# Optimization experiments

Hardware: AMD Instinct MI355X
Metric: run time of the kernel (lower is better)

## Reference

```python
import jax, jax.numpy as jnp
import numpy as np

IN, H, B = 1024, 1024, 8192
EPS = 1e-5

def _ln(x, g, b):
    mu = jnp.mean(x, axis=-1, keepdims=True)
    var = jnp.mean(jnp.square(x - mu), axis=-1, keepdims=True)
    return (x - mu) * jax.lax.rsqrt(var + EPS) * g + b

def setup_inputs() -> dict:
    key = jax.random.key(0)
    ks = jax.random.split(key, 6)
    inp = {
        "input": jax.random.normal(ks[0], (B, IN), dtype=jnp.float32),
        "h_prev": jax.random.normal(ks[1], (B, H), dtype=jnp.float32),
        "c_prev": jax.random.normal(ks[2], (B, H), dtype=jnp.float32),
        # Linear(in, 4H, bias=False) weights, stored [out, in] like torch
        "w_i": jax.random.normal(ks[3], (4 * H, IN), dtype=jnp.float32) / np.sqrt(IN),
        "w_h": jax.random.normal(ks[4], (4 * H, H), dtype=jnp.float32) / np.sqrt(H),
    }
    for name in ("ln_i", "ln_h", "ln_g", "ln_o", "ln_c"):
        inp[name + "_g"] = jnp.ones((H,), dtype=jnp.float32)
        inp[name + "_b"] = jnp.zeros((H,), dtype=jnp.float32)
    return inp

def reference(input, h_prev, c_prev, w_i, w_h,
              ln_i_g, ln_i_b, ln_h_g, ln_h_b, ln_g_g, ln_g_b,
              ln_o_g, ln_o_b, ln_c_g, ln_c_b):
    gi = input @ w_i.T            # [B, 4H]
    gh = h_prev @ w_h.T           # [B, 4H]
    i_i, i_f, i_gc, i_o = jnp.split(gi, 4, axis=-1)
    h_i, h_f, h_g, h_o = jnp.split(gh, 4, axis=-1)
    i_g = jax.nn.sigmoid(_ln(i_i + h_i, ln_i_g, ln_i_b))
    f_g = jax.nn.sigmoid(_ln(i_f + h_f, ln_h_g, ln_h_b))
    # NOTE: faithful to source bug — uses sigmoided i_g (not chunk i_gc) here
    g_g = jnp.tanh(_ln(i_g + h_g, ln_g_g, ln_g_b))
    o_g = jax.nn.sigmoid(_ln(i_o + h_o, ln_o_g, ln_o_b))
    c_new = _ln(f_g * c_prev + i_g * g_g, ln_c_g, ln_c_b)
    h_new = o_g * jnp.tanh(c_new)
    return (h_new, c_new)
```

## Files before the change

### kernel.cpp

```cpp
#include <hip/hip_runtime.h>
#include <hip/hip_bf16.h>

#define BATCH 8192
#define HDIM  1024
#define KDIM  2048
#define NDIM  4096

__device__ inline unsigned short f2bf(float x) {
    unsigned int u = __float_as_uint(x);
    unsigned int r = (u + 0x7fffu + ((u >> 16) & 1u)) >> 16;
    return (unsigned short)r;
}
__device__ inline float bf2f(unsigned short u) {
    return __uint_as_float((unsigned int)u << 16);
}

__global__ __launch_bounds__(256) void convert_kernel(
    const float* __restrict__ wi, const float* __restrict__ wh,
    const float* __restrict__ input, const float* __restrict__ h_prev,
    unsigned short* __restrict__ Wb, unsigned short* __restrict__ Xb)
{
    int idx = blockIdx.x * 256 + threadIdx.x;
    const int NW = NDIM * 512;
    float4 v;
    unsigned short* dst;
    if (idx < NW) {
        int n = idx >> 9;
        int k = (idx & 511) << 2;
        if (k < 1024) {
            if (n >= 2048 && n < 3072) v = make_float4(0.f, 0.f, 0.f, 0.f);
            else                       v = *(const float4*)(wi + (size_t)n * 1024 + k);
        } else {
            v = *(const float4*)(wh + (size_t)n * 1024 + (k - 1024));
        }
        dst = Wb + (size_t)n * KDIM + k;
    } else {
        int j = idx - NW;
        int r = j >> 9;
        int k = (j & 511) << 2;
        if (k < 1024) v = *(const float4*)(input  + (size_t)r * 1024 + k);
        else          v = *(const float4*)(h_prev + (size_t)r * 1024 + (k - 1024));
        dst = Xb + (size_t)r * KDIM + k;
    }
    ushort4 o;
    o.x = f2bf(v.x); o.y = f2bf(v.y); o.z = f2bf(v.z); o.w = f2bf(v.w);
    *(ushort4*)dst = o;
}

#define BM 256
#define BN 128
#define BK 64

typedef __attribute__((ext_vector_type(8))) short bf16x8;
typedef __attribute__((ext_vector_type(4))) float f32x4;

__global__ __launch_bounds__(512) void gemm_bt_kernel(
    const unsigned short* __restrict__ A,
    const unsigned short* __restrict__ Bw,
    unsigned short* __restrict__ G,
    int M)
{
    __shared__ unsigned short As[BM * BK];
    __shared__ unsigned short Bs[BN * BK];

    const int tid  = threadIdx.x;
    const int lane = tid & 63;
    const int wave = tid >> 6;

    const int bid = blockIdx.x;
    const int bm  = (bid >> 5) * BM;
    const int bn  = (bid & 31) * BN;

    f32x4 acc[4][4] = {};

    const int wm = (wave >> 1) * 64;
    const int wn = (wave & 1) * 64;

    const int srow = lane >> 3;
    const int c_sw = (lane & 7) ^ srow;

    int k0 = 0;
    if (bn >= 2048 && bn < 3072) k0 = 1024;

    for (; k0 < KDIM; k0 += BK) {
#pragma unroll
        for (int p = 0; p < 4; ++p) {
            const int rbase = wave * 32 + p * 8;
            const unsigned short* gA =
                A + (size_t)(bm + rbase + srow) * KDIM + k0 + c_sw * 8;
            __builtin_amdgcn_global_load_lds(
                (const __attribute__((address_space(1))) void*)gA,
                (__attribute__((address_space(3))) void*)&As[rbase * BK], 16, 0, 0);
        }
#pragma unroll
        for (int p = 0; p < 2; ++p) {
            const int rbase = wave * 16 + p * 8;
            const unsigned short* gB =
                Bw + (size_t)(bn + rbase + srow) * KDIM + k0 + c_sw * 8;
            __builtin_amdgcn_global_load_lds(
                (const __attribute__((address_space(1))) void*)gB,
                (__attribute__((address_space(3))) void*)&Bs[rbase * BK], 16, 0, 0);
        }
        __syncthreads();

#pragma unroll
        for (int kk = 0; kk < 2; ++kk) {
            bf16x8 af[4], bfr[4];
            const int cbase = kk * 4 + (lane >> 4);
#pragma unroll
            for (int i = 0; i < 4; ++i) {
                const int ra = wm + i * 16 + (lane & 15);
                af[i]  = *(const bf16x8*)&As[ra * BK + ((cbase ^ (ra & 7)) * 8)];
                const int rb = wn + i * 16 + (lane & 15);
                bfr[i] = *(const bf16x8*)&Bs[rb * BK + ((cbase ^ (rb & 7)) * 8)];
            }
#pragma unroll
            for (int i = 0; i < 4; ++i)
#pragma unroll
                for (int j = 0; j < 4; ++j)
                    acc[i][j] = __builtin_amdgcn_mfma_f32_16x16x32_bf16(
                        af[i], bfr[j], acc[i][j], 0, 0, 0);
        }
        __syncthreads();
    }

#pragma unroll
    for (int i = 0; i < 4; ++i) {
#pragma unroll
        for (int j = 0; j < 4; ++j) {
#pragma unroll
            for (int r = 0; r < 4; ++r) {
                int row = bm + wm + i * 16 + (lane >> 4) * 4 + r;
                int col = bn + wn + j * 16 + (lane & 15);
                G[(size_t)row * NDIM + col] = f2bf(acc[i][j][r]);
            }
        }
    }
}

__device__ inline float sigmoid_f(float x) { return 1.f / (1.f + __expf(-x)); }
__device__ inline float tanh_f(float x) { return 1.f - 2.f / (__expf(2.f * x) + 1.f); }

typedef __attribute__((ext_vector_type(8))) unsigned short us8;

__device__ inline void wstats(const float* x, float& mu, float& rs)
{
    float s = 0.f, q = 0.f;
#pragma unroll
    for (int e = 0; e < 16; ++e) { s += x[e]; q += x[e] * x[e]; }
#pragma unroll
    for (int o = 1; o < 64; o <<= 1) {
        s += __shfl_xor(s, o);
        q += __shfl_xor(q, o);
    }
    mu = s * (1.f / 1024.f);
    float var = q * (1.f / 1024.f) - mu * mu;
    rs = rsqrtf(var + 1e-5f);
}

#define LOADG16(dst, basep)                                            \
    _Pragma("unroll")                                                  \
    for (int j = 0; j < 2; ++j) {                                      \
        us8 t = *(const us8*)((basep) + j * 512 + cbase);              \
        _Pragma("unroll")                                              \
        for (int e = 0; e < 8; ++e) dst[j * 8 + e] = bf2f(t[e]);       \
    }

#define LOADF16(dst, basep)                                            \
    _Pragma("unroll")                                                  \
    for (int j = 0; j < 2; ++j) {                                      \
        float4 a = *(const float4*)((basep) + j * 512 + cbase);        \
        float4 b = *(const float4*)((basep) + j * 512 + cbase + 4);    \
        dst[j * 8 + 0] = a.x; dst[j * 8 + 1] = a.y;                    \
        dst[j * 8 + 2] = a.z; dst[j * 8 + 3] = a.w;                    \
        dst[j * 8 + 4] = b.x; dst[j * 8 + 5] = b.y;                    \
        dst[j * 8 + 6] = b.z; dst[j * 8 + 7] = b.w;                    \
    }

__global__ __launch_bounds__(256) void lstm_ew_kernel(
    const unsigned short* __restrict__ G,
    const float* __restrict__ c_prev,
    const float* __restrict__ p0g, const float* __restrict__ p0b,
    const float* __restrict__ p1g, const float* __restrict__ p1b,
    const float* __restrict__ p2g, const float* __restrict__ p2b,
    const float* __restrict__ p3g, const float* __restrict__ p3b,
    const float* __restrict__ p4g, const float* __restrict__ p4b,
    float* __restrict__ out_h, float* __restrict__ out_c,
    int row_base)
{
    const int lane  = threadIdx.x & 63;
    const int wave  = threadIdx.x >> 6;
    const int r     = blockIdx.x * 4 + wave;
    const int grow  = row_base + r;
    const int cbase = lane * 8;

    const unsigned short* Grow = G + (size_t)r * NDIM;

    float tmp[16], pg[16], pb[16];
    float ig[16], cm[16], og[16];
    float mu, rs;

    LOADG16(tmp, Grow);
    wstats(tmp, mu, rs);
    LOADF16(pg, p0g); LOADF16(pb, p0b);
#pragma unroll
    for (int e = 0; e < 16; ++e)
        ig[e] = sigmoid_f((tmp[e] - mu) * rs * pg[e] + pb[e]);

    LOADG16(tmp, Grow + 1024);
    wstats(tmp, mu, rs);
    LOADF16(pg, p1g); LOADF16(pb, p1b);
    LOADF16(cm, c_prev + (size_t)grow * HDIM);
#pragma unroll
    for (int e = 0; e < 16; ++e)
        cm[e] *= sigmoid_f((tmp[e] - mu) * rs * pg[e] + pb[e]);

    LOADG16(tmp, Grow + 2048);
#pragma unroll
    for (int e = 0; e < 16; ++e) tmp[e] += ig[e];
    wstats(tmp, mu, rs);
    LOADF16(pg, p2g); LOADF16(pb, p2b);
#pragma unroll
    for (int e = 0; e < 16; ++e)
        cm[e] += ig[e] * tanh_f((tmp[e] - mu) * rs * pg[e] + pb[e]);

    LOADG16(tmp, Grow + 3072);
    wstats(tmp, mu, rs);
    LOADF16(pg, p3g); LOADF16(pb, p3b);
#pragma unroll
    for (int e = 0; e < 16; ++e)
        og[e] = sigmoid_f((tmp[e] - mu) * rs * pg[e] + pb[e]);

    wstats(cm, mu, rs);
    LOADF16(pg, p4g); LOADF16(pb, p4b);
    float cn[16], hn[16];
#pragma unroll
    for (int e = 0; e < 16; ++e) {
        cn[e] = (cm[e] - mu) * rs * pg[e] + pb[e];
        hn[e] = og[e] * tanh_f(cn[e]);
    }

    float* oh = out_h + (size_t)grow * HDIM;
    float* oc = out_c + (size_t)grow * HDIM;
#pragma unroll
    for (int j = 0; j < 2; ++j) {
        *(float4*)(oh + j * 512 + cbase) =
            make_float4(hn[j*8+0], hn[j*8+1], hn[j*8+2], hn[j*8+3]);
        *(float4*)(oh + j * 512 + cbase + 4) =
            make_float4(hn[j*8+4], hn[j*8+5], hn[j*8+6], hn[j*8+7]);
        *(float4*)(oc + j * 512 + cbase) =
            make_float4(cn[j*8+0], cn[j*8+1], cn[j*8+2], cn[j*8+3]);
        *(float4*)(oc + j * 512 + cbase + 4) =
            make_float4(cn[j*8+4], cn[j*8+5], cn[j*8+6], cn[j*8+7]);
    }
}

extern "C" void kernel_launch(void* const* d_in, const int* in_sizes, int n_in,
                              void* d_out, int out_size, void* d_ws, size_t ws_size,
                              hipStream_t stream)
{
    const float* input  = (const float*)d_in[0];
    const float* h_prev = (const float*)d_in[1];
    const float* c_prev = (const float*)d_in[2];
    const float* w_i    = (const float*)d_in[3];
    const float* w_h    = (const float*)d_in[4];
    const float* lng[10];
    for (int i = 0; i < 10; ++i) lng[i] = (const float*)d_in[5 + i];

    unsigned short* Xb = (unsigned short*)d_ws;
    size_t xb_bytes = (size_t)BATCH * KDIM * 2;
    unsigned short* Wb = (unsigned short*)((char*)d_ws + xb_bytes);
    size_t wb_bytes = (size_t)NDIM * KDIM * 2;
    unsigned short* G = (unsigned short*)((char*)d_ws + xb_bytes + wb_bytes);

    size_t g_avail = (ws_size > xb_bytes + wb_bytes) ? (ws_size - xb_bytes - wb_bytes) : 0;
    long max_rows = (long)(g_avail / ((size_t)NDIM * sizeof(unsigned short)));
    int chunk = (max_rows >= BATCH) ? BATCH : (int)((max_rows / BM) * BM);
    if (chunk <= 0) chunk = BM;

    convert_kernel<<<(NDIM * 512 + BATCH * 512) / 256, 256, 0, stream>>>(
        w_i, w_h, input, h_prev, Wb, Xb);

    float* out_h = (float*)d_out;
    float* out_c = out_h + (size_t)BATCH * HDIM;

    for (int rb = 0; rb < BATCH; rb += chunk) {
        int rows = (BATCH - rb < chunk) ? (BATCH - rb) : chunk;
        gemm_bt_kernel<<<(rows / BM) * (NDIM / BN), 512, 0, stream>>>(
            Xb + (size_t)rb * KDIM, Wb, G, rows);
        lstm_ew_kernel<<<rows / 4, 256, 0, stream>>>(
            G, c_prev, lng[0], lng[1], lng[2], lng[3], lng[4],
            lng[5], lng[6], lng[7], lng[8], lng[9], out_h, out_c, rb);
    }
}
```

Before: 330.7 us.

## Double-buffer GEMM LDS tiles, widen block tile to 256x256, prioritize MFMA phases

Restructures the bf16 GEMM main loop so global-to-LDS loads for the next K tile are issued into a second LDS buffer while the current tile is computed, with an explicit vmcnt wait and raw barriers. This hides global load latency behind MFMA work. The block tile grows from 256x128 to 256x256, with each wave computing a 128x64 sub-tile to raise operand reuse. Fragment loads are interleaved with MFMA groups under s_setprio. The cost is 128KB of LDS per block, a larger accumulator register footprint and half as many blocks, which lowers occupancy and the parallelism available across CUs.

```diff
diff --git a/kernel.cpp b/kernel.cpp
--- a/kernel.cpp
+++ b/kernel.cpp
@@ -48,11 +48,83 @@
 }
 
 #define BM 256
-#define BN 128
+#define BN 256
 #define BK 64
 
 typedef __attribute__((ext_vector_type(8))) short bf16x8;
 typedef __attribute__((ext_vector_type(4))) float f32x4;
+
+#define BARRIER() { asm volatile("" ::: "memory"); \
+                    __builtin_amdgcn_s_barrier();  \
+                    asm volatile("" ::: "memory"); }
+
+#define STAGE_TILE(buf, kbase)                                                 \
+  {                                                                            \
+    _Pragma("unroll") for (int p = 0; p < 4; ++p) {                            \
+      const int rbase = wave * 32 + p * 8;                                     \
+      __builtin_amdgcn_global_load_lds(                                        \
+          (const __attribute__((address_space(1))) void*)(                     \
+              A + (size_t)(bm + rbase + srow) * KDIM + (kbase) + c_sw * 8),    \
+          (__attribute__((address_space(3))) void*)&As[buf][rbase * BK],       \
+          16, 0, 0);                                                           \
+      __builtin_amdgcn_global_load_lds(                                        \
+          (const __attribute__((address_space(1))) void*)(                     \
+              Bw + (size_t)(bn + rbase + srow) * KDIM + (kbase) + c_sw * 8),   \
+          (__attribute__((address_space(3))) void*)&Bs[buf][rbase * BK],       \
+          16, 0, 0);                                                           \
+    }                                                                          \
+  }
+
+#define COMPUTE_TILE(buf)                                                      \
+  {                                                                            \
+    const unsigned short* __restrict__ Ab = As[buf];                           \
+    const unsigned short* __restrict__ Bb = Bs[buf];                           \
+    bf16x8 a0[4][2], a1[4][2], b0[2][2], b1[2][2];                             \
+    _Pragma("unroll") for (int i = 0; i < 4; ++i)                              \
+      _Pragma("unroll") for (int kk = 0; kk < 2; ++kk)                         \
+        a0[i][kk] = *(const bf16x8*)&Ab[(wm + i * 16 + ln15) * BK +            \
+                                        (((kk * 4 + l16) ^ r7) * 8)];          \
+    _Pragma("unroll") for (int j = 0; j < 2; ++j)                              \
+      _Pragma("unroll") for (int kk = 0; kk < 2; ++kk)                         \
+        b0[j][kk] = *(const bf16x8*)&Bb[(wn + j * 16 + ln15) * BK +            \
+                                        (((kk * 4 + l16) ^ r7) * 8)];          \
+    __builtin_amdgcn_s_setprio(1);                                             \
+    _Pragma("unroll") for (int i = 0; i < 4; ++i)                              \
+      _Pragma("unroll") for (int j = 0; j < 2; ++j)                            \
+        _Pragma("unroll") for (int kk = 0; kk < 2; ++kk)                       \
+          acc[i][j] = __builtin_amdgcn_mfma_f32_16x16x32_bf16(                 \
+              a0[i][kk], b0[j][kk], acc[i][j], 0, 0, 0);                       \
+    __builtin_amdgcn_s_setprio(0);                                             \
+    _Pragma("unroll") for (int j = 0; j < 2; ++j)                              \
+      _Pragma("unroll") for (int kk = 0; kk < 2; ++kk)                         \
+        b1[j][kk] = *(const bf16x8*)&Bb[(wn + (j + 2) * 16 + ln15) * BK +      \
+                                        (((kk * 4 + l16) ^ r7) * 8)];          \
+    __builtin_amdgcn_s_setprio(1);                                             \
+    _Pragma("unroll") for (int i = 0; i < 4; ++i)                              \
+      _Pragma("unroll") for (int j = 0; j < 2; ++j)                            \
+        _Pragma("unroll") for (int kk = 0; kk < 2; ++kk)                       \
+          acc[i][j + 2] = __builtin_amdgcn_mfma_f32_16x16x32_bf16(             \
+              a0[i][kk], b1[j][kk], acc[i][j + 2], 0, 0, 0);                   \
+    __builtin_amdgcn_s_setprio(0);                                             \
+    _Pragma("unroll") for (int i = 0; i < 4; ++i)                              \
+      _Pragma("unroll") for (int kk = 0; kk < 2; ++kk)                         \
+        a1[i][kk] = *(const bf16x8*)&Ab[(wm + (i + 4) * 16 + ln15) * BK +      \
+                                        (((kk * 4 + l16) ^ r7) * 8)];          \
+    __builtin_amdgcn_s_setprio(1);                                             \
+    _Pragma("unroll") for (int i = 0; i < 4; ++i)                              \
+      _Pragma("unroll") for (int j = 0; j < 2; ++j)                            \
+        _Pragma("unroll") for (int kk = 0; kk < 2; ++kk)                       \
+          acc[i + 4][j + 2] = __builtin_amdgcn_mfma_f32_16x16x32_bf16(         \
+              a1[i][kk], b1[j][kk], acc[i + 4][j + 2], 0, 0, 0);               \
+    __builtin_amdgcn_s_setprio(0);                                             \
+    __builtin_amdgcn_s_setprio(1);                                             \
+    _Pragma("unroll") for (int i = 0; i < 4; ++i)                              \
+      _Pragma("unroll") for (int j = 0; j < 2; ++j)                            \
+        _Pragma("unroll") for (int kk = 0; kk < 2; ++kk)                       \
+          acc[i + 4][j] = __builtin_amdgcn_mfma_f32_16x16x32_bf16(             \
+              a1[i][kk], b0[j][kk], acc[i + 4][j], 0, 0, 0);                   \
+    __builtin_amdgcn_s_setprio(0);                                             \
+  }
 
 __global__ __launch_bounds__(512) void gemm_bt_kernel(
     const unsigned short* __restrict__ A,
@@ -60,78 +132,55 @@
     unsigned short* __restrict__ G,
     int M)
 {
-    __shared__ unsigned short As[BM * BK];
-    __shared__ unsigned short Bs[BN * BK];
+    __shared__ unsigned short As[2][BM * BK];
+    __shared__ unsigned short Bs[2][BN * BK];
 
     const int tid  = threadIdx.x;
     const int lane = tid & 63;
     const int wave = tid >> 6;
 
     const int bid = blockIdx.x;
-    const int bm  = (bid >> 5) * BM;
-    const int bn  = (bid & 31) * BN;
-
-    f32x4 acc[4][4] = {};
-
-    const int wm = (wave >> 1) * 64;
-    const int wn = (wave & 1) * 64;
+    const int bm  = (bid >> 4) * BM;
+    const int bn  = (bid & 15) * BN;
+
+    const int wm = (wave >> 2) * 128;
+    const int wn = (wave & 3) * 64;
 
     const int srow = lane >> 3;
     const int c_sw = (lane & 7) ^ srow;
 
+    const int ln15 = lane & 15;
+    const int l16  = lane >> 4;
+    const int r7   = lane & 7;
+
+    f32x4 acc[8][4] = {};
+
     int k0 = 0;
     if (bn >= 2048 && bn < 3072) k0 = 1024;
-
-    for (; k0 < KDIM; k0 += BK) {
-#pragma unroll
-        for (int p = 0; p < 4; ++p) {
-            const int rbase = wave * 32 + p * 8;
-            const unsigned short* gA =
-                A + (size_t)(bm + rbase + srow) * KDIM + k0 + c_sw * 8;
-            __builtin_amdgcn_global_load_lds(
-                (const __attribute__((address_space(1))) void*)gA,
-                (__attribute__((address_space(3))) void*)&As[rbase * BK], 16, 0, 0);
-        }
-#pragma unroll
-        for (int p = 0; p < 2; ++p) {
-            const int rbase = wave * 16 + p * 8;
-            const unsigned short* gB =
-                Bw + (size_t)(bn + rbase + srow) * KDIM + k0 + c_sw * 8;
-            __builtin_amdgcn_global_load_lds(
-                (const __attribute__((address_space(1))) void*)gB,
-                (__attribute__((address_space(3))) void*)&Bs[rbase * BK], 16, 0, 0);
-        }
-        __syncthreads();
-
-#pragma unroll
-        for (int kk = 0; kk < 2; ++kk) {
-            bf16x8 af[4], bfr[4];
-            const int cbase = kk * 4 + (lane >> 4);
-#pragma unroll
-            for (int i = 0; i < 4; ++i) {
-                const int ra = wm + i * 16 + (lane & 15);
-                af[i]  = *(const bf16x8*)&As[ra * BK + ((cbase ^ (ra & 7)) * 8)];
-                const int rb = wn + i * 16 + (lane & 15);
-                bfr[i] = *(const bf16x8*)&Bs[rb * BK + ((cbase ^ (rb & 7)) * 8)];
-            }
-#pragma unroll
-            for (int i = 0; i < 4; ++i)
-#pragma unroll
-                for (int j = 0; j < 4; ++j)
-                    acc[i][j] = __builtin_amdgcn_mfma_f32_16x16x32_bf16(
-                        af[i], bfr[j], acc[i][j], 0, 0, 0);
-        }
-        __syncthreads();
-    }
-
-#pragma unroll
-    for (int i = 0; i < 4; ++i) {
+    const int nt = (KDIM - k0) / BK;
+
+    STAGE_TILE(0, k0);
+    int cur = 0;
+    for (int t = 0; t < nt - 1; ++t) {
+        STAGE_TILE(cur ^ 1, k0 + (t + 1) * BK);
+        asm volatile("s_waitcnt vmcnt(8)" ::: "memory");
+        BARRIER();
+        COMPUTE_TILE(cur);
+        BARRIER();
+        cur ^= 1;
+    }
+    asm volatile("s_waitcnt vmcnt(0)" ::: "memory");
+    BARRIER();
+    COMPUTE_TILE(cur);
+
+#pragma unroll
+    for (int i = 0; i < 8; ++i) {
 #pragma unroll
         for (int j = 0; j < 4; ++j) {
 #pragma unroll
             for (int r = 0; r < 4; ++r) {
-                int row = bm + wm + i * 16 + (lane >> 4) * 4 + r;
-                int col = bn + wn + j * 16 + (lane & 15);
+                int row = bm + wm + i * 16 + l16 * 4 + r;
+                int col = bn + wn + j * 16 + ln15;
                 G[(size_t)row * NDIM + col] = f2bf(acc[i][j][r]);
             }
         }
```

Result: slower. 352.7 us (+6.6%).

## Triple-buffer GEMM LDS tiles with async prefetch two stages ahead

Applied to the files above, without the earlier changes.

Replaces the single-buffered load-sync-compute loop in the bf16 MFMA GEMM with a three-stage LDS ring. Global-to-LDS loads for tile t+2 are interleaved with the MFMA work on tile t, using explicit vmcnt waits and a single barrier per iteration. MFMA sections also raise wave priority via s_setprio. This hides global load latency behind compute, at the cost of three times the LDS (144KB), which may limit occupancy to one block per CU.

```diff
diff --git a/kernel.cpp b/kernel.cpp
--- a/kernel.cpp
+++ b/kernel.cpp
@@ -54,14 +54,65 @@
 typedef __attribute__((ext_vector_type(8))) short bf16x8;
 typedef __attribute__((ext_vector_type(4))) float f32x4;
 
+#define BARRIER() { asm volatile("" ::: "memory"); \
+                    __builtin_amdgcn_s_barrier();  \
+                    asm volatile("" ::: "memory"); }
+
+#define STAGE_A3(buf, kbase)                                                   \
+  {                                                                            \
+    _Pragma("unroll") for (int p = 0; p < 3; ++p) {                            \
+      const int rbase = wave * 32 + p * 8;                                     \
+      __builtin_amdgcn_global_load_lds(                                        \
+          (const __attribute__((address_space(1))) void*)(                     \
+              A + (size_t)(bm + rbase + srow) * KDIM + (kbase) + c_sw * 8),    \
+          (__attribute__((address_space(3))) void*)&As[buf][rbase * BK],       \
+          16, 0, 0);                                                           \
+    }                                                                          \
+  }
+#define STAGE_B3(buf, kbase)                                                   \
+  {                                                                            \
+    const int rbase = wave * 32 + 24;                                          \
+    __builtin_amdgcn_global_load_lds(                                          \
+        (const __attribute__((address_space(1))) void*)(                       \
+            A + (size_t)(bm + rbase + srow) * KDIM + (kbase) + c_sw * 8),      \
+        (__attribute__((address_space(3))) void*)&As[buf][rbase * BK],         \
+        16, 0, 0);                                                             \
+    _Pragma("unroll") for (int p = 0; p < 2; ++p) {                            \
+      const int rb2 = wave * 16 + p * 8;                                       \
+      __builtin_amdgcn_global_load_lds(                                        \
+          (const __attribute__((address_space(1))) void*)(                     \
+              Bw + (size_t)(bn + rb2 + srow) * KDIM + (kbase) + c_sw * 8),     \
+          (__attribute__((address_space(3))) void*)&Bs[buf][rb2 * BK],         \
+          16, 0, 0);                                                           \
+    }                                                                          \
+  }
+
+#define COMPUTE_KK(cur, kk)                                                    \
+  {                                                                            \
+    bf16x8 af[4], bfr[4];                                                      \
+    const int cbase = (kk) * 4 + l16;                                          \
+    _Pragma("unroll") for (int i = 0; i < 4; ++i) {                            \
+      const int ra = wm + i * 16 + ln15;                                       \
+      af[i]  = *(const bf16x8*)&As[cur][ra * BK + ((cbase ^ (ra & 7)) * 8)];   \
+      const int rb = wn + i * 16 + ln15;                                       \
+      bfr[i] = *(const bf16x8*)&Bs[cur][rb * BK + ((cbase ^ (rb & 7)) * 8)];   \
+    }                                                                          \
+    __builtin_amdgcn_s_setprio(1);                                             \
+    _Pragma("unroll") for (int i = 0; i < 4; ++i)                              \
+      _Pragma("unroll") for (int j = 0; j < 4; ++j)                            \
+        acc[i][j] = __builtin_amdgcn_mfma_f32_16x16x32_bf16(                   \
+            af[i], bfr[j], acc[i][j], 0, 0, 0);                                \
+    __builtin_amdgcn_s_setprio(0);                                             \
+  }
+
 __global__ __launch_bounds__(512) void gemm_bt_kernel(
     const unsigned short* __restrict__ A,
     const unsigned short* __restrict__ Bw,
     unsigned short* __restrict__ G,
     int M)
 {
-    __shared__ unsigned short As[BM * BK];
-    __shared__ unsigned short Bs[BN * BK];
+    __shared__ unsigned short As[3][BM * BK];
+    __shared__ unsigned short Bs[3][BN * BK];
 
     const int tid  = threadIdx.x;
     const int lane = tid & 63;
@@ -71,57 +122,43 @@
     const int bm  = (bid >> 5) * BM;
     const int bn  = (bid & 31) * BN;
 
-    f32x4 acc[4][4] = {};
-
     const int wm = (wave >> 1) * 64;
     const int wn = (wave & 1) * 64;
 
     const int srow = lane >> 3;
     const int c_sw = (lane & 7) ^ srow;
 
+    const int ln15 = lane & 15;
+    const int l16  = lane >> 4;
+
+    f32x4 acc[4][4] = {};
+
     int k0 = 0;
     if (bn >= 2048 && bn < 3072) k0 = 1024;
-
-    for (; k0 < KDIM; k0 += BK) {
-#pragma unroll
-        for (int p = 0; p < 4; ++p) {
-            const int rbase = wave * 32 + p * 8;
-            const unsigned short* gA =
-                A + (size_t)(bm + rbase + srow) * KDIM + k0 + c_sw * 8;
-            __builtin_amdgcn_global_load_lds(
-                (const __attribute__((address_space(1))) void*)gA,
-                (__attribute__((address_space(3))) void*)&As[rbase * BK], 16, 0, 0);
+    const int nt = (KDIM - k0) / BK;
+
+    STAGE_A3(0, k0); STAGE_B3(0, k0);
+    STAGE_A3(1, k0 + BK); STAGE_B3(1, k0 + BK);
+    asm volatile("s_waitcnt vmcnt(6)" ::: "memory");
+    BARRIER();
+
+    int cur = 0;
+    int sb  = 2;
+    for (int t = 0; t < nt; ++t) {
+        const int kpre = k0 + (t + 2) * BK;
+        const bool pf = (t + 2 < nt);
+        if (pf) STAGE_A3(sb, kpre);
+        COMPUTE_KK(cur, 0);
+        if (pf) STAGE_B3(sb, kpre);
+        COMPUTE_KK(cur, 1);
+        if (pf) {
+            asm volatile("s_waitcnt vmcnt(6)" ::: "memory");
+        } else if (t + 1 < nt) {
+            asm volatile("s_waitcnt vmcnt(0)" ::: "memory");
         }
-#pragma unroll
-        for (int p = 0; p < 2; ++p) {
-            const int rbase = wave * 16 + p * 8;
-            const unsigned short* gB =
-                Bw + (size_t)(bn + rbase + srow) * KDIM + k0 + c_sw * 8;
-            __builtin_amdgcn_global_load_lds(
-                (const __attribute__((address_space(1))) void*)gB,
-                (__attribute__((address_space(3))) void*)&Bs[rbase * BK], 16, 0, 0);
-        }
-        __syncthreads();
-
-#pragma unroll
-        for (int kk = 0; kk < 2; ++kk) {
-            bf16x8 af[4], bfr[4];
-            const int cbase = kk * 4 + (lane >> 4);
-#pragma unroll
-            for (int i = 0; i < 4; ++i) {
-                const int ra = wm + i * 16 + (lane & 15);
-                af[i]  = *(const bf16x8*)&As[ra * BK + ((cbase ^ (ra & 7)) * 8)];
-                const int rb = wn + i * 16 + (lane & 15);
-                bfr[i] = *(const bf16x8*)&Bs[rb * BK + ((cbase ^ (rb & 7)) * 8)];
-            }
-#pragma unroll
-            for (int i = 0; i < 4; ++i)
-#pragma unroll
-                for (int j = 0; j < 4; ++j)
-                    acc[i][j] = __builtin_amdgcn_mfma_f32_16x16x32_bf16(
-                        af[i], bfr[j], acc[i][j], 0, 0, 0);
-        }
-        __syncthreads();
+        if (t + 1 < nt) BARRIER();
+        cur = (cur == 2) ? 0 : cur + 1;
+        sb  = (sb  == 2) ? 0 : sb + 1;
     }
 
 #pragma unroll
@@ -130,8 +167,8 @@
         for (int j = 0; j < 4; ++j) {
 #pragma unroll
             for (int r = 0; r < 4; ++r) {
-                int row = bm + wm + i * 16 + (lane >> 4) * 4 + r;
-                int col = bn + wn + j * 16 + (lane & 15);
+                int row = bm + wm + i * 16 + l16 * 4 + r;
+                int col = bn + wn + j * 16 + ln15;
                 G[(size_t)row * NDIM + col] = f2bf(acc[i][j][r]);
             }
         }
```

Measured after the change: 410.3 us. 24.1% more time.
